# Kernel tuning notes

Hardware: AMD Instinct MI355X
Metric: run time of the kernel (lower is better)

## Reference

```python
import jax, jax.numpy as jnp
import numpy as np

V, D, C, H = 32, 128, 2048, 8
B, M = 8, 2048
HD = D // H


def rms_norm(x, scale):
    # Whole-tensor (per-batch) RMS over dims (1,2), as in the source (quirky but faithful).
    Bx, Mx, Dx = x.shape
    fr = jnp.sqrt(jnp.sum(x * x, axis=(1, 2))) * (Mx * Dx) ** -0.5  # (B,)
    raw = x / fr[:, None, None]
    return scale[:Mx, :][None, :, :] * raw


def rope_tables(Mx):
    i = jnp.arange(D // 2, dtype=jnp.float32)
    # NOTE: faithful to source: exponent uses (i-1), not i.
    base = jnp.power(10000.0, -2.0 * (i - 1.0) / D)  # (D/2,)
    pos = jnp.arange(Mx, dtype=jnp.float32)
    ang = pos[:, None] * base[None, :]  # (M, D/2)
    return jnp.cos(ang), jnp.sin(ang)


def apply_rope(t, cos, sin):
    # Equivalent to bmm with the block-diagonal 2x2 rotation matrices:
    # out[2i]   =  t[2i]*cos + t[2i+1]*sin
    # out[2i+1] = -t[2i]*sin + t[2i+1]*cos
    te, to = t[..., 0::2], t[..., 1::2]
    oe = te * cos + to * sin
    oo = -te * sin + to * cos
    return jnp.stack([oe, oo], axis=-1).reshape(t.shape)


def mha(q, k, v, in_w, in_b, out_w, out_b):
    Bx, Mx, _ = q.shape
    qp = q @ in_w[:D].T + in_b[:D]
    kp = k @ in_w[D:2 * D].T + in_b[D:2 * D]
    vp = v @ in_w[2 * D:].T + in_b[2 * D:]
    qh = qp.reshape(Bx, Mx, H, HD).transpose(0, 2, 1, 3)
    kh = kp.reshape(Bx, Mx, H, HD).transpose(0, 2, 1, 3)
    vh = vp.reshape(Bx, Mx, H, HD).transpose(0, 2, 1, 3)
    scores = jnp.einsum('bhqd,bhkd->bhqk', qh, kh) / jnp.sqrt(jnp.float32(HD))
    causal = jnp.tril(jnp.ones((Mx, Mx), dtype=bool))
    scores = jnp.where(causal[None, None], scores, -jnp.inf)
    probs = jax.nn.softmax(scores, axis=-1)  # dropout=0.1 in train mode; eval here
    o = jnp.einsum('bhqk,bhkd->bhqd', probs, vh)
    o = o.transpose(0, 2, 1, 3).reshape(Bx, Mx, D)
    return o @ out_w.T + out_b


def setup_inputs():
    key = jax.random.key(0)
    ks = jax.random.split(key, 12)
    s = 0.02
    return {
        'idx': jax.random.randint(ks[0], (B, M), 0, V),
        'targets': jax.random.randint(ks[1], (B, M), 0, V),
        'emb': jax.random.normal(ks[2], (V, D), jnp.float32) * s,
        'rms_scale': jnp.ones((C, D), jnp.float32),
        'Wq': jax.random.normal(ks[3], (D, D), jnp.float32) * s,
        'Wk': jax.random.normal(ks[4], (D, D), jnp.float32) * s,
        'Wv': jax.random.normal(ks[5], (D, D), jnp.float32) * s,
        'in_proj_w': jax.random.normal(ks[6], (3 * D, D), jnp.float32) * s,
        'in_proj_b': jnp.zeros((3 * D,), jnp.float32),
        'out_proj_w': jax.random.normal(ks[7], (D, D), jnp.float32) * s,
        'out_proj_b': jnp.zeros((D,), jnp.float32),
        'lin_w': jax.random.normal(ks[8], (D, D), jnp.float32) * s,
        'lin_b': jnp.zeros((D,), jnp.float32),
        'out_w': jax.random.normal(ks[9], (V, D), jnp.float32) * s,
        'out_b': jnp.zeros((V,), jnp.float32),
    }


def reference(idx, targets, emb, rms_scale, Wq, Wk, Wv, in_proj_w, in_proj_b,
              out_proj_w, out_proj_b, lin_w, lin_b, out_w, out_b):
    x = emb[idx]                                  # (B, M, D)
    x = rms_norm(x, rms_scale)
    Q = x @ Wq.T
    K = x @ Wk.T
    Vv = x @ Wv.T
    cos, sin = rope_tables(x.shape[1])
    q_out = apply_rope(Q, cos, sin)
    k_out = apply_rope(K, cos, sin)
    v_out = apply_rope(Vv, cos, sin)              # source rotates V too (faithful)
    x = x + mha(q_out, k_out, v_out, in_proj_w, in_proj_b, out_proj_w, out_proj_b)
    x = rms_norm(x, rms_scale)
    x = x + jax.nn.relu(x @ lin_w.T + lin_b)
    logits = x @ out_w.T + out_b                  # (B, M, V)
    logp = jax.nn.log_softmax(logits, axis=-1)
    nll = -jnp.take_along_axis(logp, targets[..., None], axis=-1)[..., 0]
    loss = jnp.mean(nll)
    return logits, loss
```

## Files before the change

kernel.cpp:

```cpp
#include <hip/hip_runtime.h>
#include <hip/hip_bf16.h>
#include <math.h>

#define Vv   32
#define Dd   128
#define Hh   8
#define Bb   8
#define Mm   2048
#define BM   (Bb*Mm)
#define NEL  (BM*Dd)
#define XNS  140
#define QKS  396

typedef _Float16 half4_t __attribute__((ext_vector_type(4)));
typedef _Float16 half8_t __attribute__((ext_vector_type(8)));
typedef __fp16   fp16x2  __attribute__((ext_vector_type(2)));
typedef float    float4_t __attribute__((ext_vector_type(4)));
#define MFMA16 __builtin_amdgcn_mfma_f32_16x16x16f16

#if __has_builtin(__builtin_amdgcn_exp2f)
__device__ __forceinline__ float fexp2(float x) { return __builtin_amdgcn_exp2f(x); }
#else
__device__ __forceinline__ float fexp2(float x) { return __expf(x * 0.6931471805599453f); }
#endif

__global__ __launch_bounds__(256) void prep_kernel(const float* __restrict__ Wq,
                                                   const float* __restrict__ Wk,
                                                   const float* __restrict__ Wv,
                                                   const float* __restrict__ in_w,
                                                   const float* __restrict__ out_pw,
                                                   const float* __restrict__ lin_w,
                                                   const float* __restrict__ out_w,
                                                   _Float16* __restrict__ Wh,
                                                   float* __restrict__ cosT,
                                                   float* __restrict__ sinT) {
    int gid = blockIdx.x * 256 + threadIdx.x;
    if (gid < 135168) {
        const float* src;
        int i;
        if (gid < 131072) {
            int seg = gid >> 14; i = gid & 16383;
            src = seg == 0 ? Wq : seg == 1 ? Wk : seg == 2 ? Wv :
                  seg < 6 ? in_w + (size_t)(seg - 3) * 16384 :
                  seg == 6 ? out_pw : lin_w;
        } else { src = out_w; i = gid - 131072; }
        int tile = i >> 8, within = i & 255;
        int nt = tile >> 3, kk = tile & 7;
        int r = within >> 4, cc = within & 15;
        Wh[gid] = (_Float16)src[(nt * 16 + r) * 128 + kk * 16 + cc];
    } else {
        int rid = gid - 135168;
        int i = rid & 63, m = rid >> 6;
        float ex = -2.0f * ((float)i - 1.0f) / 128.0f;
        float basef = expf(ex * 9.210340371976184f);
        float ang = (float)m * basef;
        cosT[rid] = cosf(ang);
        sinT[rid] = sinf(ang);
    }
}

__global__ __launch_bounds__(256) void gather_sumsq_kernel(const int* __restrict__ idx,
                                                           const float* __restrict__ emb,
                                                           _Float16* __restrict__ Xh,
                                                           float* __restrict__ partials) {
    int gid = blockIdx.x * 256 + threadIdx.x;
    int token = gid >> 5, t4 = gid & 31;
    float4 x = *(const float4*)(emb + (size_t)idx[token] * 128 + t4 * 4);
    half4_t o;
    o[0] = (_Float16)x.x; o[1] = (_Float16)x.y; o[2] = (_Float16)x.z; o[3] = (_Float16)x.w;
    *(half4_t*)(Xh + (size_t)gid * 4) = o;
    float v = x.x * x.x + x.y * x.y + x.z * x.z + x.w * x.w;
    #pragma unroll
    for (int off = 32; off; off >>= 1) v += __shfl_xor(v, off);
    __shared__ float wsum[4];
    int lane = threadIdx.x & 63, wave = threadIdx.x >> 6;
    if (lane == 0) wsum[wave] = v;
    __syncthreads();
    if (threadIdx.x == 0) partials[blockIdx.x] = wsum[0] + wsum[1] + wsum[2] + wsum[3];
}

__global__ __launch_bounds__(256) void ssq_reduce_kernel(const float* __restrict__ partials,
                                                         int count,
                                                         float* __restrict__ inv) {
    int b = blockIdx.x, t = threadIdx.x;
    float v = (t < count) ? partials[b * count + t] : 0.f;
    #pragma unroll
    for (int off = 32; off; off >>= 1) v += __shfl_xor(v, off);
    __shared__ float wsum[4];
    int lane = t & 63, wave = t >> 6;
    if (lane == 0) wsum[wave] = v;
    __syncthreads();
    if (t == 0) inv[b] = 512.0f / sqrtf(wsum[0] + wsum[1] + wsum[2] + wsum[3]);
}

__global__ __launch_bounds__(256) void normscale_f_kernel(const float* __restrict__ X,
                                                          const float* __restrict__ scale,
                                                          const float* __restrict__ inv,
                                                          _Float16* __restrict__ outh) {
    int gid = blockIdx.x * 256 + threadIdx.x;
    float iv = inv[gid >> 16];
    const float* sp = scale + (size_t)((gid >> 5) & 2047) * 128 + (gid & 31) * 4;
    float4 s4 = *(const float4*)sp;
    float4 x = *(const float4*)(X + (size_t)gid * 4);
    half4_t o;
    o[0] = (_Float16)(x.x * iv * s4.x);
    o[1] = (_Float16)(x.y * iv * s4.y);
    o[2] = (_Float16)(x.z * iv * s4.z);
    o[3] = (_Float16)(x.w * iv * s4.w);
    *(half4_t*)(outh + (size_t)gid * 4) = o;
}

__global__ __launch_bounds__(256) void gemm_qkvproj_kernel(const _Float16* __restrict__ xh,
                                                           const float* __restrict__ scale,
                                                           const float* __restrict__ inv,
                                                           const _Float16* __restrict__ Whqkv,
                                                           const _Float16* __restrict__ Whin,
                                                           const float* __restrict__ in_b,
                                                           const float* __restrict__ cosT,
                                                           const float* __restrict__ sinT,
                                                           _Float16* __restrict__ xnh,
                                                           _Float16* __restrict__ Qp,
                                                           _Float16* __restrict__ Kp,
                                                           _Float16* __restrict__ Vp) {
    __shared__ _Float16 xn[32 * XNS];
    __shared__ _Float16 qkv[32 * QKS];
    int tid = threadIdx.x;
    int row0 = blockIdx.x * 32;
    {
        float iv = inv[row0 >> 11];
        #pragma unroll
        for (int it = 0; it < 2; it++) {
            int idx = tid + it * 256;
            int rw = idx >> 4, c8 = (idx & 15) * 8;
            int m = (row0 + rw) & (Mm - 1);
            half8_t x8 = *(const half8_t*)(xh + (size_t)(row0 + rw) * 128 + c8);
            const float* sp = scale + (size_t)m * 128 + c8;
            float4 s0 = *(const float4*)sp;
            float4 s1 = *(const float4*)(sp + 4);
            half8_t o8;
            o8[0] = (_Float16)((float)x8[0] * iv * s0.x);
            o8[1] = (_Float16)((float)x8[1] * iv * s0.y);
            o8[2] = (_Float16)((float)x8[2] * iv * s0.z);
            o8[3] = (_Float16)((float)x8[3] * iv * s0.w);
            o8[4] = (_Float16)((float)x8[4] * iv * s1.x);
            o8[5] = (_Float16)((float)x8[5] * iv * s1.y);
            o8[6] = (_Float16)((float)x8[6] * iv * s1.z);
            o8[7] = (_Float16)((float)x8[7] * iv * s1.w);
            *(half8_t*)(xn + rw * XNS + c8) = o8;
            *(half8_t*)(xnh + (size_t)(row0 + rw) * 128 + c8) = o8;
        }
    }
    __syncthreads();
    int wave = tid >> 6, lane = tid & 63;
    int r = lane & 15, c = lane >> 4;
    int lofs = r * 16 + 4 * c;
    int nb = wave * 96;
    int nb16 = wave * 6;
    {
        half4_t af[2][8];
        #pragma unroll
        for (int rt = 0; rt < 2; rt++)
            #pragma unroll
            for (int kk = 0; kk < 8; kk++)
                af[rt][kk] = *(const half4_t*)(xn + (rt * 16 + r) * XNS + kk * 16 + 4 * c);
        float4_t acc[2][6];
        #pragma unroll
        for (int rt = 0; rt < 2; rt++)
            #pragma unroll
            for (int t = 0; t < 6; t++) acc[rt][t] = (float4_t){0.f, 0.f, 0.f, 0.f};
        #pragma unroll
        for (int kk = 0; kk < 8; kk++) {
            half4_t wf[6];
            #pragma unroll
            for (int t = 0; t < 6; t++)
                wf[t] = *(const half4_t*)(Whqkv + ((nb16 + t) * 8 + kk) * 256 + lofs);
            #pragma unroll
            for (int t = 0; t < 6; t++) {
                acc[0][t] = MFMA16(af[0][kk], wf[t], acc[0][t], 0, 0, 0);
                acc[1][t] = MFMA16(af[1][kk], wf[t], acc[1][t], 0, 0, 0);
            }
        }
        #pragma unroll
        for (int rt = 0; rt < 2; rt++) {
            #pragma unroll
            for (int t = 0; t < 6; t++) {
                int n = nb + t * 16 + r;
                int ci = (n & 127) >> 1;
                #pragma unroll
                for (int reg = 0; reg < 4; reg++) {
                    int m2 = (row0 + rt * 16 + 4 * c + reg) & (Mm - 1);
                    float v = acc[rt][t][reg];
                    float vp = __shfl_xor(v, 1);
                    float cs = cosT[m2 * 64 + ci], sn = sinT[m2 * 64 + ci];
                    v = (n & 1) ? (-vp * sn + v * cs) : (v * cs + vp * sn);
                    qkv[(rt * 16 + 4 * c + reg) * QKS + n] = (_Float16)v;
                }
            }
        }
    }
    __syncthreads();
    {
        int seg_lo = nb >> 7;
        int seg_hi = (nb + 80) >> 7;
        half4_t aql[2][8], aqh[2][8];
        #pragma unroll
        for (int rt = 0; rt < 2; rt++)
            #pragma unroll
            for (int kk = 0; kk < 8; kk++) {
                aql[rt][kk] = *(const half4_t*)(qkv + (rt * 16 + r) * QKS + seg_lo * 128 + kk * 16 + 4 * c);
                aqh[rt][kk] = *(const half4_t*)(qkv + (rt * 16 + r) * QKS + seg_hi * 128 + kk * 16 + 4 * c);
            }
        float4_t acc[2][6];
        #pragma unroll
        for (int rt = 0; rt < 2; rt++)
            #pragma unroll
            for (int t = 0; t < 6; t++) acc[rt][t] = (float4_t){0.f, 0.f, 0.f, 0.f};
        #pragma unroll
        for (int kk = 0; kk < 8; kk++) {
            half4_t wf[6];
            #pragma unroll
            for (int t = 0; t < 6; t++) {
                int colg = nb + t * 16;
                int seg = colg >> 7;
                int ntl = (colg & 127) >> 4;
                wf[t] = *(const half4_t*)(Whin + ((seg * 8 + ntl) * 8 + kk) * 256 + lofs);
            }
            #pragma unroll
            for (int t = 0; t < 6; t++) {
                int seg = (nb + t * 16) >> 7;
                acc[0][t] = MFMA16(seg == seg_lo ? aql[0][kk] : aqh[0][kk], wf[t], acc[0][t], 0, 0, 0);
                acc[1][t] = MFMA16(seg == seg_lo ? aql[1][kk] : aqh[1][kk], wf[t], acc[1][t], 0, 0, 0);
            }
        }
        int bb = row0 >> 11;
        #pragma unroll
        for (int rt = 0; rt < 2; rt++) {
            int t16 = ((row0 + rt * 16) & 2047) >> 4;
            #pragma unroll
            for (int t = 0; t < 6; t++) {
                int colg = nb + t * 16;
                int seg = colg >> 7;
                int h = (colg & 127) >> 4;
                size_t tb = ((size_t)(bb * 8 + h) * 128 + t16) * 256;
                float bv = in_b[colg + r];
                _Float16* dst = seg == 0 ? Qp : seg == 1 ? Kp : Vp;
                #pragma unroll
                for (int reg = 0; reg < 4; reg++) {
                    float v = acc[rt][t][reg] + bv;
                    int key = 4 * c + reg;
                    if (seg < 2) dst[tb + key * 16 + r] = (_Float16)v;
                    else         dst[tb + r * 16 + key] = (_Float16)v;
                }
            }
        }
    }
}

__global__ __launch_bounds__(256) void gemm_ep1_kernel(const _Float16* __restrict__ Oh,
                                                       const _Float16* __restrict__ W6,
                                                       const float* __restrict__ bias,
                                                       const _Float16* __restrict__ xnh,
                                                       float* __restrict__ xres,
                                                       float* __restrict__ partials) {
    __shared__ _Float16 At[32 * XNS];
    int tid = threadIdx.x;
    int row0 = blockIdx.x * 32;
    #pragma unroll
    for (int it = 0; it < 2; it++) {
        int idx = tid + it * 256;
        int rw = idx >> 4, c8 = (idx & 15) * 8;
        *(half8_t*)(At + rw * XNS + c8) = *(const half8_t*)(Oh + (size_t)(row0 + rw) * 128 + c8);
    }
    __syncthreads();
    int wave = tid >> 6, lane = tid & 63;
    int r = lane & 15, c = lane >> 4;
    int lofs = r * 16 + 4 * c;
    int n0 = wave * 32;
    half4_t af[2][8];
    #pragma unroll
    for (int rt = 0; rt < 2; rt++)
        #pragma unroll
        for (int kk = 0; kk < 8; kk++)
            af[rt][kk] = *(const half4_t*)(At + (rt * 16 + r) * XNS + kk * 16 + 4 * c);
    float4_t acc[2][2];
    #pragma unroll
    for (int rt = 0; rt < 2; rt++) {
        acc[rt][0] = (float4_t){0.f, 0.f, 0.f, 0.f};
        acc[rt][1] = (float4_t){0.f, 0.f, 0.f, 0.f};
    }
    #pragma unroll
    for (int kk = 0; kk < 8; kk++) {
        half4_t wf[2];
        wf[0] = *(const half4_t*)(W6 + ((wave * 2 + 0) * 8 + kk) * 256 + lofs);
        wf[1] = *(const half4_t*)(W6 + ((wave * 2 + 1) * 8 + kk) * 256 + lofs);
        #pragma unroll
        for (int t = 0; t < 2; t++) {
            acc[0][t] = MFMA16(af[0][kk], wf[t], acc[0][t], 0, 0, 0);
            acc[1][t] = MFMA16(af[1][kk], wf[t], acc[1][t], 0, 0, 0);
        }
    }
    float lssq = 0.f;
    #pragma unroll
    for (int rt = 0; rt < 2; rt++) {
        #pragma unroll
        for (int t = 0; t < 2; t++) {
            int n = n0 + t * 16 + r;
            float bv = bias[n];
            #pragma unroll
            for (int reg = 0; reg < 4; reg++) {
                int row = row0 + rt * 16 + 4 * c + reg;
                float v = acc[rt][t][reg] + bv + (float)xnh[(size_t)row * 128 + n];
                lssq += v * v;
                xres[(size_t)row * 128 + n] = v;
            }
        }
    }
    #pragma unroll
    for (int off = 32; off; off >>= 1) lssq += __shfl_xor(lssq, off);
    __shared__ float wsum[4];
    if (lane == 0) wsum[wave] = lssq;
    __syncthreads();
    if (tid == 0) partials[blockIdx.x] = wsum[0] + wsum[1] + wsum[2] + wsum[3];
}

__global__ __launch_bounds__(256) void gemm_ep2_kernel(const _Float16* __restrict__ Ah,
                                                       const _Float16* __restrict__ W7,
                                                       const float* __restrict__ bias,
                                                       const float* __restrict__ xres,
                                                       _Float16* __restrict__ ffoh) {
    __shared__ _Float16 At[32 * XNS];
    int tid = threadIdx.x;
    int row0 = blockIdx.x * 32;
    #pragma unroll
    for (int it = 0; it < 2; it++) {
        int idx = tid + it * 256;
        int rw = idx >> 4, c8 = (idx & 15) * 8;
        *(half8_t*)(At + rw * XNS + c8) = *(const half8_t*)(Ah + (size_t)(row0 + rw) * 128 + c8);
    }
    __syncthreads();
    int wave = tid >> 6, lane = tid & 63;
    int r = lane & 15, c = lane >> 4;
    int lofs = r * 16 + 4 * c;
    int n0 = wave * 32;
    half4_t af[2][8];
    #pragma unroll
    for (int rt = 0; rt < 2; rt++)
        #pragma unroll
        for (int kk = 0; kk < 8; kk++)
            af[rt][kk] = *(const half4_t*)(At + (rt * 16 + r) * XNS + kk * 16 + 4 * c);
    float4_t acc[2][2];
    #pragma unroll
    for (int rt = 0; rt < 2; rt++) {
        acc[rt][0] = (float4_t){0.f, 0.f, 0.f, 0.f};
        acc[rt][1] = (float4_t){0.f, 0.f, 0.f, 0.f};
    }
    #pragma unroll
    for (int kk = 0; kk < 8; kk++) {
        half4_t wf[2];
        wf[0] = *(const half4_t*)(W7 + ((wave * 2 + 0) * 8 + kk) * 256 + lofs);
        wf[1] = *(const half4_t*)(W7 + ((wave * 2 + 1) * 8 + kk) * 256 + lofs);
        #pragma unroll
        for (int t = 0; t < 2; t++) {
            acc[0][t] = MFMA16(af[0][kk], wf[t], acc[0][t], 0, 0, 0);
            acc[1][t] = MFMA16(af[1][kk], wf[t], acc[1][t], 0, 0, 0);
        }
    }
    #pragma unroll
    for (int rt = 0; rt < 2; rt++) {
        #pragma unroll
        for (int t = 0; t < 2; t++) {
            int n = n0 + t * 16 + r;
            float bv = bias[n];
            #pragma unroll
            for (int reg = 0; reg < 4; reg++) {
                int row = row0 + rt * 16 + 4 * c + reg;
                float v = fmaxf(acc[rt][t][reg] + bv, 0.f) + xres[(size_t)row * 128 + n];
                ffoh[(size_t)row * 128 + n] = (_Float16)v;
            }
        }
    }
}

__device__ __forceinline__ half4_t attn_exps(float4_t st, float& ls) {
    float p0 = fexp2(st[0]), p1 = fexp2(st[1]);
    float p2 = fexp2(st[2]), p3 = fexp2(st[3]);
    ls += (p0 + p1) + (p2 + p3);
    fp16x2 lo = __builtin_amdgcn_cvt_pkrtz(p0, p1);
    fp16x2 hi = __builtin_amdgcn_cvt_pkrtz(p2, p3);
    half4_t pf;
    pf[0] = (_Float16)lo[0]; pf[1] = (_Float16)lo[1];
    pf[2] = (_Float16)hi[0]; pf[3] = (_Float16)hi[1];
    return pf;
}
__device__ __forceinline__ half4_t attn_exps_masked(float4_t st, float& ls, int r, int c) {
    float p0 = (4 * c + 0 <= r) ? fexp2(st[0]) : 0.f;
    float p1 = (4 * c + 1 <= r) ? fexp2(st[1]) : 0.f;
    float p2 = (4 * c + 2 <= r) ? fexp2(st[2]) : 0.f;
    float p3 = (4 * c + 3 <= r) ? fexp2(st[3]) : 0.f;
    ls += (p0 + p1) + (p2 + p3);
    fp16x2 lo = __builtin_amdgcn_cvt_pkrtz(p0, p1);
    fp16x2 hi = __builtin_amdgcn_cvt_pkrtz(p2, p3);
    half4_t pf;
    pf[0] = (_Float16)lo[0]; pf[1] = (_Float16)lo[1];
    pf[2] = (_Float16)hi[0]; pf[3] = (_Float16)hi[1];
    return pf;
}

__global__ __launch_bounds__(256) void attn_kernel(const _Float16* __restrict__ Qp,
                                                   const _Float16* __restrict__ Kp,
                                                   const _Float16* __restrict__ Vp,
                                                   _Float16* __restrict__ Oh) {
    int wave = threadIdx.x >> 6, lane = threadIdx.x & 63;
    int wid = blockIdx.x * 4 + wave;
    int qa = wid & 63, bh = wid >> 6, qb = 127 - qa;
    int r = lane & 15, c = lane >> 4;
    int lofs = r * 16 + 4 * c;
    const _Float16* Kb = Kp + (size_t)bh * 32768 + lofs;
    const _Float16* Vb = Vp + (size_t)bh * 32768 + lofs;
    const _Float16* Qb = Qp + (size_t)bh * 32768 + lofs;
    half4_t qfa = *(const half4_t*)(Qb + qa * 256);
    half4_t qfb = *(const half4_t*)(Qb + qb * 256);
    const _Float16 qscale = (_Float16)0.36067376f;
    qfa *= qscale;
    qfb *= qscale;
    float4_t zero = {0.f, 0.f, 0.f, 0.f};
    float4_t oa = zero, ob = zero;
    float lsa = 0.f, lsb = 0.f;

    int kt = 0;
    for (; kt + 2 <= qa; kt += 2) {
        half4_t k0 = *(const half4_t*)(Kb + kt * 256);
        half4_t v0 = *(const half4_t*)(Vb + kt * 256);
        half4_t k1 = *(const half4_t*)(Kb + kt * 256 + 256);
        half4_t v1 = *(const half4_t*)(Vb + kt * 256 + 256);
        float4_t s0a = MFMA16(k0, qfa, zero, 0, 0, 0);
        float4_t s0b = MFMA16(k0, qfb, zero, 0, 0, 0);
        float4_t s1a = MFMA16(k1, qfa, zero, 0, 0, 0);
        float4_t s1b = MFMA16(k1, qfb, zero, 0, 0, 0);
        half4_t p0a = attn_exps(s0a, lsa);
        half4_t p0b = attn_exps(s0b, lsb);
        half4_t p1a = attn_exps(s1a, lsa);
        half4_t p1b = attn_exps(s1b, lsb);
        oa = MFMA16(p0a, v0, oa, 0, 0, 0);
        ob = MFMA16(p0b, v0, ob, 0, 0, 0);
        oa = MFMA16(p1a, v1, oa, 0, 0, 0);
        ob = MFMA16(p1b, v1, ob, 0, 0, 0);
    }
    if (kt < qa) {
        half4_t k0 = *(const half4_t*)(Kb + kt * 256);
        half4_t v0 = *(const half4_t*)(Vb + kt * 256);
        float4_t sa = MFMA16(k0, qfa, zero, 0, 0, 0);
        float4_t sb = MFMA16(k0, qfb, zero, 0, 0, 0);
        half4_t pa = attn_exps(sa, lsa);
        half4_t pb = attn_exps(sb, lsb);
        oa = MFMA16(pa, v0, oa, 0, 0, 0);
        ob = MFMA16(pb, v0, ob, 0, 0, 0);
    }
    {
        half4_t k0 = *(const half4_t*)(Kb + qa * 256);
        half4_t v0 = *(const half4_t*)(Vb + qa * 256);
        float4_t sa = MFMA16(k0, qfa, zero, 0, 0, 0);
        float4_t sb = MFMA16(k0, qfb, zero, 0, 0, 0);
        half4_t pa = attn_exps_masked(sa, lsa, r, c);
        half4_t pb = attn_exps(sb, lsb);
        oa = MFMA16(pa, v0, oa, 0, 0, 0);
        ob = MFMA16(pb, v0, ob, 0, 0, 0);
    }
    for (kt = qa + 1; kt + 2 <= qb; kt += 2) {
        half4_t k0 = *(const half4_t*)(Kb + kt * 256);
        half4_t v0 = *(const half4_t*)(Vb + kt * 256);
        half4_t k1 = *(const half4_t*)(Kb + kt * 256 + 256);
        half4_t v1 = *(const half4_t*)(Vb + kt * 256 + 256);
        float4_t s0 = MFMA16(k0, qfb, zero, 0, 0, 0);
        float4_t s1 = MFMA16(k1, qfb, zero, 0, 0, 0);
        half4_t p0 = attn_exps(s0, lsb);
        half4_t p1 = attn_exps(s1, lsb);
        ob = MFMA16(p0, v0, ob, 0, 0, 0);
        ob = MFMA16(p1, v1, ob, 0, 0, 0);
    }
    {
        half4_t k0 = *(const half4_t*)(Kb + qb * 256);
        half4_t v0 = *(const half4_t*)(Vb + qb * 256);
        float4_t sb = MFMA16(k0, qfb, zero, 0, 0, 0);
        half4_t pb = attn_exps_masked(sb, lsb, r, c);
        ob = MFMA16(pb, v0, ob, 0, 0, 0);
    }
    lsa += __shfl_xor(lsa, 16); lsa += __shfl_xor(lsa, 32);
    lsb += __shfl_xor(lsb, 16); lsb += __shfl_xor(lsb, 32);
    int b = bh >> 3, h = bh & 7;
    #pragma unroll
    for (int reg = 0; reg < 4; reg++) {
        float la = __shfl(lsa, 4 * c + reg);
        float lb = __shfl(lsb, 4 * c + reg);
        Oh[(size_t)(b * Mm + qa * 16 + 4 * c + reg) * 128 + h * 16 + r] = (_Float16)(oa[reg] / la);
        Oh[(size_t)(b * Mm + qb * 16 + 4 * c + reg) * 128 + h * 16 + r] = (_Float16)(ob[reg] / lb);
    }
}

__global__ __launch_bounds__(256) void logits_loss_kernel(const _Float16* __restrict__ Xh,
                                                          const _Float16* __restrict__ Wo16,
                                                          const float* __restrict__ bo,
                                                          const int* __restrict__ targets,
                                                          float* __restrict__ logits,
                                                          float* __restrict__ nllBuf) {
    __shared__ _Float16 At[64 * XNS];
    int tid = threadIdx.x;
    int rowb = blockIdx.x * 64;
    #pragma unroll
    for (int it = 0; it < 4; it++) {
        int idx = tid + it * 256;
        int rw = idx >> 4, c8 = (idx & 15) * 8;
        *(half8_t*)(At + rw * XNS + c8) = *(const half8_t*)(Xh + (size_t)(rowb + rw) * 128 + c8);
    }
    __syncthreads();
    int wave = tid >> 6, lane = tid & 63;
    int r = lane & 15, c = lane >> 4;
    int lofs = r * 16 + 4 * c;
    int row0 = rowb + wave * 16;
    half4_t af[8];
    #pragma unroll
    for (int kk = 0; kk < 8; kk++)
        af[kk] = *(const half4_t*)(At + (wave * 16 + r) * XNS + kk * 16 + 4 * c);
    float4_t acc[2];
    acc[0] = (float4_t){0.f, 0.f, 0.f, 0.f};
    acc[1] = (float4_t){0.f, 0.f, 0.f, 0.f};
    #pragma unroll
    for (int kk = 0; kk < 8; kk++) {
        #pragma unroll
        for (int t = 0; t < 2; t++) {
            half4_t wf = *(const half4_t*)(Wo16 + (t * 8 + kk) * 256 + lofs);
            acc[t] = MFMA16(af[kk], wf, acc[t], 0, 0, 0);
        }
    }
    float b0 = bo[r], b1 = bo[r + 16];
    #pragma unroll
    for (int reg = 0; reg < 4; reg++) {
        int row = row0 + 4 * c + reg;
        float l0 = acc[0][reg] + b0;
        float l1 = acc[1][reg] + b1;
        logits[(size_t)row * 32 + r] = l0;
        logits[(size_t)row * 32 + 16 + r] = l1;
        float mx = fmaxf(l0, l1);
        #pragma unroll
        for (int off = 8; off; off >>= 1) mx = fmaxf(mx, __shfl_xor(mx, off));
        float se = __expf(l0 - mx) + __expf(l1 - mx);
        #pragma unroll
        for (int off = 8; off; off >>= 1) se += __shfl_xor(se, off);
        int tgt = targets[row];
        float sel = (tgt & 16) ? l1 : l0;
        float tval = __shfl(sel, (lane & 48) | (tgt & 15));
        if (r == 0) nllBuf[row] = logf(se) + mx - tval;
    }
}

__global__ __launch_bounds__(256) void loss_reduce_kernel(const float* __restrict__ nllBuf,
                                                          float* __restrict__ out) {
    int t = threadIdx.x;
    double s = 0.0;
    #pragma unroll
    for (int i = 0; i < 64; i++) s += (double)nllBuf[t * 64 + i];
    __shared__ double sh[256];
    sh[t] = s;
    __syncthreads();
    for (int off = 128; off; off >>= 1) {
        if (t < off) sh[t] += sh[t + off];
        __syncthreads();
    }
    if (t == 0) out[0] = (float)(sh[0] * (1.0 / (double)BM));
}

extern "C" void kernel_launch(void* const* d_in, const int* in_sizes, int n_in,
                              void* d_out, int out_size, void* d_ws, size_t ws_size,
                              hipStream_t stream) {
    const int*   idx       = (const int*)d_in[0];
    const int*   targets   = (const int*)d_in[1];
    const float* emb       = (const float*)d_in[2];
    const float* rms_scale = (const float*)d_in[3];
    const float* Wq        = (const float*)d_in[4];
    const float* Wk        = (const float*)d_in[5];
    const float* Wv        = (const float*)d_in[6];
    const float* in_w      = (const float*)d_in[7];
    const float* in_b      = (const float*)d_in[8];
    const float* out_pw    = (const float*)d_in[9];
    const float* out_pb    = (const float*)d_in[10];
    const float* lin_w     = (const float*)d_in[11];
    const float* lin_b     = (const float*)d_in[12];
    const float* out_w     = (const float*)d_in[13];
    const float* out_b     = (const float*)d_in[14];
    float* out = (float*)d_out;

    char* base = (char*)d_ws;
    const size_t MB = 1024 * 1024;
    _Float16* xh16  = (_Float16*)base;
    _Float16* xnh   = (_Float16*)(base + 4 * MB);
    _Float16* Oh    = (_Float16*)(base + 8 * MB);
    _Float16* x2nh  = (_Float16*)(base + 12 * MB);
    _Float16* ffoh  = (_Float16*)(base + 16 * MB);
    _Float16* Qp    = (_Float16*)(base + 20 * MB);
    _Float16* Kp    = (_Float16*)(base + 24 * MB);
    _Float16* Vp    = (_Float16*)(base + 28 * MB);
    float*    xres  = (float*)(base + 32 * MB);
    float*    cosT  = (float*)(base + 40 * MB);
    float*    sinT  = cosT + Mm * 64;
    float*    part1 = sinT + Mm * 64;
    float*    part2 = part1 + 2048;
    float*    inv1  = part2 + 512;
    float*    inv2  = inv1 + 8;
    _Float16* Wh    = (_Float16*)(inv2 + 8);
    float*    nllBuf = (float*)(Wh + 135168);

    prep_kernel<<<1040, 256, 0, stream>>>(Wq, Wk, Wv, in_w, out_pw, lin_w, out_w, Wh, cosT, sinT);
    gather_sumsq_kernel<<<NEL / 1024, 256, 0, stream>>>(idx, emb, xh16, part1);
    ssq_reduce_kernel<<<8, 256, 0, stream>>>(part1, 256, inv1);

    gemm_qkvproj_kernel<<<BM / 32, 256, 0, stream>>>(xh16, rms_scale, inv1,
                                                     Wh, Wh + 3 * 16384, in_b,
                                                     cosT, sinT, xnh, Qp, Kp, Vp);

    attn_kernel<<<64 * 64 / 4, 256, 0, stream>>>(Qp, Kp, Vp, Oh);

    gemm_ep1_kernel<<<BM / 32, 256, 0, stream>>>(Oh, Wh + 6 * 16384, out_pb, xnh, xres, part2);
    ssq_reduce_kernel<<<8, 256, 0, stream>>>(part2, 64, inv2);
    normscale_f_kernel<<<NEL / 1024, 256, 0, stream>>>(xres, rms_scale, inv2, x2nh);
    gemm_ep2_kernel<<<BM / 32, 256, 0, stream>>>(x2nh, Wh + 7 * 16384, lin_b, xres, ffoh);

    logits_loss_kernel<<<BM / 64, 256, 0, stream>>>(ffoh, Wh + 131072, out_b, targets, out, nllBuf);
    loss_reduce_kernel<<<1, 256, 0, stream>>>(nllBuf, out + (size_t)BM * Vv);
}
```

Baseline: 175.2 us.

## Fold RMS partial reductions into consumers, prefetch K/V in attention loop

Drops the two small ssq_reduce launches: each consumer block (qkv projection and normscale) now re-reduces the per-batch partial sums itself and computes the inverse RMS inline. The attention loop is restructured into a single unified loop with register double-buffered K/V prefetch and per-tile masking branches. Softmax row sums are accumulated with fp16 dot2 instructions on the packed probabilities. This removes launch overhead and aims to hide load latency, at the cost of redundant reduction work per block and extra branches inside the attention loop.

```diff
diff --git a/kernel.cpp b/kernel.cpp
--- a/kernel.cpp
+++ b/kernel.cpp
@@ -79,26 +79,16 @@
     if (threadIdx.x == 0) partials[blockIdx.x] = wsum[0] + wsum[1] + wsum[2] + wsum[3];
 }
 
-__global__ __launch_bounds__(256) void ssq_reduce_kernel(const float* __restrict__ partials,
-                                                         int count,
-                                                         float* __restrict__ inv) {
-    int b = blockIdx.x, t = threadIdx.x;
-    float v = (t < count) ? partials[b * count + t] : 0.f;
-    #pragma unroll
-    for (int off = 32; off; off >>= 1) v += __shfl_xor(v, off);
-    __shared__ float wsum[4];
-    int lane = t & 63, wave = t >> 6;
-    if (lane == 0) wsum[wave] = v;
-    __syncthreads();
-    if (t == 0) inv[b] = 512.0f / sqrtf(wsum[0] + wsum[1] + wsum[2] + wsum[3]);
-}
-
 __global__ __launch_bounds__(256) void normscale_f_kernel(const float* __restrict__ X,
                                                           const float* __restrict__ scale,
-                                                          const float* __restrict__ inv,
+                                                          const float* __restrict__ part2,
                                                           _Float16* __restrict__ outh) {
     int gid = blockIdx.x * 256 + threadIdx.x;
-    float iv = inv[gid >> 16];
+    int b = gid >> 16;
+    float pv = part2[b * 64 + (threadIdx.x & 63)];
+    #pragma unroll
+    for (int off = 32; off; off >>= 1) pv += __shfl_xor(pv, off);
+    float iv = 512.0f / sqrtf(pv);
     const float* sp = scale + (size_t)((gid >> 5) & 2047) * 128 + (gid & 31) * 4;
     float4 s4 = *(const float4*)sp;
     float4 x = *(const float4*)(X + (size_t)gid * 4);
@@ -112,7 +102,7 @@
 
 __global__ __launch_bounds__(256) void gemm_qkvproj_kernel(const _Float16* __restrict__ xh,
                                                            const float* __restrict__ scale,
-                                                           const float* __restrict__ inv,
+                                                           const float* __restrict__ part1,
                                                            const _Float16* __restrict__ Whqkv,
                                                            const _Float16* __restrict__ Whin,
                                                            const float* __restrict__ in_b,
@@ -124,10 +114,18 @@
                                                            _Float16* __restrict__ Vp) {
     __shared__ _Float16 xn[32 * XNS];
     __shared__ _Float16 qkv[32 * QKS];
+    __shared__ float wsum0[4];
     int tid = threadIdx.x;
     int row0 = blockIdx.x * 32;
     {
-        float iv = inv[row0 >> 11];
+        float v = part1[(row0 >> 11) * 256 + tid];
+        #pragma unroll
+        for (int off = 32; off; off >>= 1) v += __shfl_xor(v, off);
+        if ((tid & 63) == 0) wsum0[tid >> 6] = v;
+    }
+    __syncthreads();
+    float iv = 512.0f / sqrtf(wsum0[0] + wsum0[1] + wsum0[2] + wsum0[3]);
+    {
         #pragma unroll
         for (int it = 0; it < 2; it++) {
             int idx = tid + it * 256;
@@ -384,9 +382,15 @@
 __device__ __forceinline__ half4_t attn_exps(float4_t st, float& ls) {
     float p0 = fexp2(st[0]), p1 = fexp2(st[1]);
     float p2 = fexp2(st[2]), p3 = fexp2(st[3]);
-    ls += (p0 + p1) + (p2 + p3);
     fp16x2 lo = __builtin_amdgcn_cvt_pkrtz(p0, p1);
     fp16x2 hi = __builtin_amdgcn_cvt_pkrtz(p2, p3);
+#if __has_builtin(__builtin_amdgcn_fdot2)
+    fp16x2 one2 = {(__fp16)1.0f, (__fp16)1.0f};
+    ls = __builtin_amdgcn_fdot2(lo, one2, ls, false);
+    ls = __builtin_amdgcn_fdot2(hi, one2, ls, false);
+#else
+    ls += (p0 + p1) + (p2 + p3);
+#endif
     half4_t pf;
     pf[0] = (_Float16)lo[0]; pf[1] = (_Float16)lo[1];
     pf[2] = (_Float16)hi[0]; pf[3] = (_Float16)hi[1];
@@ -397,9 +401,15 @@
     float p1 = (4 * c + 1 <= r) ? fexp2(st[1]) : 0.f;
     float p2 = (4 * c + 2 <= r) ? fexp2(st[2]) : 0.f;
     float p3 = (4 * c + 3 <= r) ? fexp2(st[3]) : 0.f;
-    ls += (p0 + p1) + (p2 + p3);
     fp16x2 lo = __builtin_amdgcn_cvt_pkrtz(p0, p1);
     fp16x2 hi = __builtin_amdgcn_cvt_pkrtz(p2, p3);
+#if __has_builtin(__builtin_amdgcn_fdot2)
+    fp16x2 one2 = {(__fp16)1.0f, (__fp16)1.0f};
+    ls = __builtin_amdgcn_fdot2(lo, one2, ls, false);
+    ls = __builtin_amdgcn_fdot2(hi, one2, ls, false);
+#else
+    ls += (p0 + p1) + (p2 + p3);
+#endif
     half4_t pf;
     pf[0] = (_Float16)lo[0]; pf[1] = (_Float16)lo[1];
     pf[2] = (_Float16)hi[0]; pf[3] = (_Float16)hi[1];
@@ -426,64 +436,43 @@
     float4_t zero = {0.f, 0.f, 0.f, 0.f};
     float4_t oa = zero, ob = zero;
     float lsa = 0.f, lsb = 0.f;
-
-    int kt = 0;
-    for (; kt + 2 <= qa; kt += 2) {
-        half4_t k0 = *(const half4_t*)(Kb + kt * 256);
-        half4_t v0 = *(const half4_t*)(Vb + kt * 256);
-        half4_t k1 = *(const half4_t*)(Kb + kt * 256 + 256);
-        half4_t v1 = *(const half4_t*)(Vb + kt * 256 + 256);
-        float4_t s0a = MFMA16(k0, qfa, zero, 0, 0, 0);
-        float4_t s0b = MFMA16(k0, qfb, zero, 0, 0, 0);
-        float4_t s1a = MFMA16(k1, qfa, zero, 0, 0, 0);
-        float4_t s1b = MFMA16(k1, qfb, zero, 0, 0, 0);
-        half4_t p0a = attn_exps(s0a, lsa);
-        half4_t p0b = attn_exps(s0b, lsb);
-        half4_t p1a = attn_exps(s1a, lsa);
-        half4_t p1b = attn_exps(s1b, lsb);
-        oa = MFMA16(p0a, v0, oa, 0, 0, 0);
-        ob = MFMA16(p0b, v0, ob, 0, 0, 0);
-        oa = MFMA16(p1a, v1, oa, 0, 0, 0);
-        ob = MFMA16(p1b, v1, ob, 0, 0, 0);
-    }
-    if (kt < qa) {
-        half4_t k0 = *(const half4_t*)(Kb + kt * 256);
-        half4_t v0 = *(const half4_t*)(Vb + kt * 256);
-        float4_t sa = MFMA16(k0, qfa, zero, 0, 0, 0);
-        float4_t sb = MFMA16(k0, qfb, zero, 0, 0, 0);
-        half4_t pa = attn_exps(sa, lsa);
-        half4_t pb = attn_exps(sb, lsb);
-        oa = MFMA16(pa, v0, oa, 0, 0, 0);
-        ob = MFMA16(pb, v0, ob, 0, 0, 0);
-    }
-    {
-        half4_t k0 = *(const half4_t*)(Kb + qa * 256);
-        half4_t v0 = *(const half4_t*)(Vb + qa * 256);
-        float4_t sa = MFMA16(k0, qfa, zero, 0, 0, 0);
-        float4_t sb = MFMA16(k0, qfb, zero, 0, 0, 0);
-        half4_t pa = attn_exps_masked(sa, lsa, r, c);
-        half4_t pb = attn_exps(sb, lsb);
-        oa = MFMA16(pa, v0, oa, 0, 0, 0);
-        ob = MFMA16(pb, v0, ob, 0, 0, 0);
-    }
-    for (kt = qa + 1; kt + 2 <= qb; kt += 2) {
-        half4_t k0 = *(const half4_t*)(Kb + kt * 256);
-        half4_t v0 = *(const half4_t*)(Vb + kt * 256);
-        half4_t k1 = *(const half4_t*)(Kb + kt * 256 + 256);
-        half4_t v1 = *(const half4_t*)(Vb + kt * 256 + 256);
-        float4_t s0 = MFMA16(k0, qfb, zero, 0, 0, 0);
-        float4_t s1 = MFMA16(k1, qfb, zero, 0, 0, 0);
-        half4_t p0 = attn_exps(s0, lsb);
-        half4_t p1 = attn_exps(s1, lsb);
-        ob = MFMA16(p0, v0, ob, 0, 0, 0);
-        ob = MFMA16(p1, v1, ob, 0, 0, 0);
-    }
-    {
-        half4_t k0 = *(const half4_t*)(Kb + qb * 256);
-        half4_t v0 = *(const half4_t*)(Vb + qb * 256);
-        float4_t sb = MFMA16(k0, qfb, zero, 0, 0, 0);
-        half4_t pb = attn_exps_masked(sb, lsb, r, c);
-        ob = MFMA16(pb, v0, ob, 0, 0, 0);
+    int nt = qb + 1;
+
+    half4_t k0 = *(const half4_t*)(Kb);
+    half4_t v0 = *(const half4_t*)(Vb);
+    half4_t k1 = *(const half4_t*)(Kb + 256);
+    half4_t v1 = *(const half4_t*)(Vb + 256);
+    for (int kt = 0; kt < nt; kt += 2) {
+        half4_t kn0 = k0, vn0 = v0, kn1 = k1, vn1 = v1;
+        if (kt + 2 < nt) {
+            kn0 = *(const half4_t*)(Kb + (size_t)(kt + 2) * 256);
+            vn0 = *(const half4_t*)(Vb + (size_t)(kt + 2) * 256);
+        }
+        if (kt + 3 < nt) {
+            kn1 = *(const half4_t*)(Kb + (size_t)(kt + 3) * 256);
+            vn1 = *(const half4_t*)(Vb + (size_t)(kt + 3) * 256);
+        }
+        {
+            float4_t sb = MFMA16(k0, qfb, zero, 0, 0, 0);
+            if (kt <= qa) {
+                float4_t sa = MFMA16(k0, qfa, zero, 0, 0, 0);
+                half4_t pa = (kt == qa) ? attn_exps_masked(sa, lsa, r, c) : attn_exps(sa, lsa);
+                oa = MFMA16(pa, v0, oa, 0, 0, 0);
+            }
+            half4_t pb = (kt == qb) ? attn_exps_masked(sb, lsb, r, c) : attn_exps(sb, lsb);
+            ob = MFMA16(pb, v0, ob, 0, 0, 0);
+        }
+        if (kt + 1 < nt) {
+            float4_t sb = MFMA16(k1, qfb, zero, 0, 0, 0);
+            if (kt + 1 <= qa) {
+                float4_t sa = MFMA16(k1, qfa, zero, 0, 0, 0);
+                half4_t pa = (kt + 1 == qa) ? attn_exps_masked(sa, lsa, r, c) : attn_exps(sa, lsa);
+                oa = MFMA16(pa, v1, oa, 0, 0, 0);
+            }
+            half4_t pb = (kt + 1 == qb) ? attn_exps_masked(sb, lsb, r, c) : attn_exps(sb, lsb);
+            ob = MFMA16(pb, v1, ob, 0, 0, 0);
+        }
+        k0 = kn0; v0 = vn0; k1 = kn1; v1 = vn1;
     }
     lsa += __shfl_xor(lsa, 16); lsa += __shfl_xor(lsa, 32);
     lsb += __shfl_xor(lsb, 16); lsb += __shfl_xor(lsb, 32);
@@ -604,24 +593,20 @@
     float*    sinT  = cosT + Mm * 64;
     float*    part1 = sinT + Mm * 64;
     float*    part2 = part1 + 2048;
-    float*    inv1  = part2 + 512;
-    float*    inv2  = inv1 + 8;
-    _Float16* Wh    = (_Float16*)(inv2 + 8);
+    _Float16* Wh    = (_Float16*)(part2 + 512);
     float*    nllBuf = (float*)(Wh + 135168);
 
     prep_kernel<<<1040, 256, 0, stream>>>(Wq, Wk, Wv, in_w, out_pw, lin_w, out_w, Wh, cosT, sinT);
     gather_sumsq_kernel<<<NEL / 1024, 256, 0, stream>>>(idx, emb, xh16, part1);
-    ssq_reduce_kernel<<<8, 256, 0, stream>>>(part1, 256, inv1);
-
-    gemm_qkvproj_kernel<<<BM / 32, 256, 0, stream>>>(xh16, rms_scale, inv1,
+
+    gemm_qkvproj_kernel<<<BM / 32, 256, 0, stream>>>(xh16, rms_scale, part1,
                                                      Wh, Wh + 3 * 16384, in_b,
                                                      cosT, sinT, xnh, Qp, Kp, Vp);
 
     attn_kernel<<<64 * 64 / 4, 256, 0, stream>>>(Qp, Kp, Vp, Oh);
 
     gemm_ep1_kernel<<<BM / 32, 256, 0, stream>>>(Oh, Wh + 6 * 16384, out_pb, xnh, xres, part2);
-    ssq_reduce_kernel<<<8, 256, 0, stream>>>(part2, 64, inv2);
-    normscale_f_kernel<<<NEL / 1024, 256, 0, stream>>>(xres, rms_scale, inv2, x2nh);
+    normscale_f_kernel<<<NEL / 1024, 256, 0, stream>>>(xres, rms_scale, part2, x2nh);
     gemm_ep2_kernel<<<BM / 32, 256, 0, stream>>>(x2nh, Wh + 7 * 16384, lin_b, xres, ffoh);
 
     logits_loss_kernel<<<BM / 64, 256, 0, stream>>>(ffoh, Wh + 131072, out_b, targets, out, nllBuf);
```

After: 181.4 us. +3.5%, slower.
